# Kernel tuning notes

Hardware: AMD Instinct MI355X
Metric: run time of the kernel (lower is better)

## Reference

```python
import jax, jax.numpy as jnp
import numpy as np

N, D, EDIM, E, K = 10000, 64, 16, 320000, 16


def _lin(key, o, i):
    # kaiming-normal-ish init, std = sqrt(2/fan_in)
    return jax.random.normal(key, (o, i), dtype=jnp.float32) * (2.0 / i) ** 0.5


def setup_inputs() -> dict:
    key = jax.random.key(0)
    ks = jax.random.split(key, 20)
    inp = {
        "x": jax.random.normal(ks[0], (N, D), dtype=jnp.float32),
        "edge_index": jax.random.randint(ks[1], (2, E), 0, N),
        "edge_attr": jax.random.normal(ks[2], (E, EDIM), dtype=jnp.float32),
        "location_info": jax.random.uniform(ks[3], (N, 4), dtype=jnp.float32),
        "k": K,
    }
    i = 4
    for name in ["sg1", "sg2", "sg3"]:
        inp[name + "_wm"] = _lin(ks[i], D, EDIM + D); i += 1
        inp[name + "_bm"] = jnp.zeros((D,), jnp.float32)
        inp[name + "_wu"] = _lin(ks[i], D, D); i += 1
        inp[name + "_bu"] = jnp.zeros((D,), jnp.float32)
    for name in ["dg1", "dg2"]:
        inp[name + "_w1"] = _lin(ks[i], 2 * D, 2 * D); i += 1
        inp[name + "_b1"] = jnp.zeros((2 * D,), jnp.float32)
        inp[name + "_w2"] = _lin(ks[i], D, 2 * D); i += 1
        inp[name + "_b2"] = jnp.zeros((D,), jnp.float32)
    inp["f1_w"] = _lin(ks[i], D, 5 * D); i += 1
    inp["f1_b"] = jnp.zeros((D,), jnp.float32)
    inp["f2_w"] = _lin(ks[i], D, 6 * D); i += 1
    inp["f2_b"] = jnp.zeros((D,), jnp.float32)
    return inp


def _knn_edges(loc, k, n):
    # dynamic kNN on location_info (euclidean, directed src->dst, with self loops)
    loc = jax.lax.stop_gradient(loc)
    d2 = jnp.sum((loc[:, None, :] - loc[None, :, :]) ** 2, axis=-1)  # [N, N]
    d2 = jnp.where(jnp.eye(n, dtype=bool), jnp.inf, d2)
    _, idx = jax.lax.top_k(-d2, k)               # idx[i] = k nearest sources of target i
    dst = jnp.repeat(jnp.arange(n), k)
    src = idx.reshape(-1)
    loops = jnp.arange(n)
    return jnp.concatenate([src, loops]), jnp.concatenate([dst, loops])


def _forward(x, edge_index, edge_attr, location_info, k,
             sg1_wm, sg1_bm, sg1_wu, sg1_bu,
             sg2_wm, sg2_bm, sg2_wu, sg2_bu,
             sg3_wm, sg3_bm, sg3_wu, sg3_bu,
             dg1_w1, dg1_b1, dg1_w2, dg1_b2,
             dg2_w1, dg2_b1, dg2_w2, dg2_b2,
             f1_w, f1_b, f2_w, f2_b):
    n = x.shape[0]
    relu = jax.nn.relu
    s_src, s_dst = edge_index[0], edge_index[1]  # PyG: row=source j, col=target i

    def static_conv(h, wm, bm, wu, bu):
        m = relu(jnp.concatenate([edge_attr, h[s_src] - h[s_dst]], axis=1) @ wm.T + bm)
        agg = jax.ops.segment_max(m, s_dst, num_segments=n)
        agg = jnp.where(jnp.isfinite(agg), agg, 0.0)  # empty segments -> 0
        return relu(agg @ wu.T + bu)

    d_src, d_dst = _knn_edges(location_info, k, n)

    def dyn_conv(h, w1, b1, w2, b2):
        xi = h[d_dst]
        xj = h[d_src]
        m = relu(relu(jnp.concatenate([xi, xj - xi], axis=1) @ w1.T + b1) @ w2.T + b2)
        return jax.ops.segment_max(m, d_dst, num_segments=n)  # self loops => no empty segments

    h1 = static_conv(x, sg1_wm, sg1_bm, sg1_wu, sg1_bu)
    h2 = static_conv(h1, sg2_wm, sg2_bm, sg2_wu, sg2_bu)
    h3 = static_conv(h2, sg3_wm, sg3_bm, sg3_wu, sg3_bu)
    g1 = dyn_conv(h1, dg1_w1, dg1_b1, dg1_w2, dg1_b2)
    g2 = dyn_conv(g1, dg2_w1, dg2_b1, dg2_w2, dg2_b2)

    cat1 = jnp.concatenate([h1, g1, g2, h2, h3], axis=1)        # [N, 5D]
    fuse1 = relu(cat1 @ f1_w.T + f1_b)                          # [N, D]
    cat2 = jnp.concatenate([fuse1, cat1], axis=1)               # [N, 6D]
    return cat2 @ f2_w.T + f2_b                                 # [N, D]


def reference(x, edge_index, edge_attr, location_info, k,
              sg1_wm, sg1_bm, sg1_wu, sg1_bu,
              sg2_wm, sg2_bm, sg2_wu, sg2_bu,
              sg3_wm, sg3_bm, sg3_wu, sg3_bu,
              dg1_w1, dg1_b1, dg1_w2, dg1_b2,
              dg2_w1, dg2_b1, dg2_w2, dg2_b2,
              f1_w, f1_b, f2_w, f2_b):
    return _forward(x, edge_index, edge_attr, location_info, k,
                    sg1_wm, sg1_bm, sg1_wu, sg1_bu,
                    sg2_wm, sg2_bm, sg2_wu, sg2_bu,
                    sg3_wm, sg3_bm, sg3_wu, sg3_bu,
                    dg1_w1, dg1_b1, dg1_w2, dg1_b2,
                    dg2_w1, dg2_b1, dg2_w2, dg2_b2,
                    f1_w, f1_b, f2_w, f2_b)
```

## Files before the change

kernel.cpp:

```cpp
#include <hip/hip_runtime.h>

#define INF_F __builtin_inff()

typedef __attribute__((ext_vector_type(8))) short short8v;
typedef __attribute__((ext_vector_type(4))) float f32x4;
typedef unsigned long long ull;

__device__ __forceinline__ short f2bf(float x) {
  const unsigned u = __float_as_uint(x);
  return (short)((u + 0x7FFFu + ((u >> 16) & 1u)) >> 16);
}

__device__ __forceinline__ unsigned mbcnt64(ull m) {
  return __builtin_amdgcn_mbcnt_hi((unsigned)(m >> 32),
                                   __builtin_amdgcn_mbcnt_lo((unsigned)m, 0u));
}

#define KNN_G 5
#define KNN_NC (KNN_G*KNN_G*KNN_G*KNN_G)
#define KNN_PCAP 1600

__global__ __launch_bounds__(256) void count2_kernel(
    const float* __restrict__ loc, int* __restrict__ cellcount,
    int* __restrict__ cellid, int n,
    const int* __restrict__ dst, int* __restrict__ deg, int E)
{
  const int i = blockIdx.x * 256 + threadIdx.x;
  if (i < n) {
    const float4 l = *(const float4*)(loc + (size_t)i*4);
    const int cx = min(KNN_G-1, (int)(l.x * (float)KNN_G));
    const int cy = min(KNN_G-1, (int)(l.y * (float)KNN_G));
    const int cz = min(KNN_G-1, (int)(l.z * (float)KNN_G));
    const int cw = min(KNN_G-1, (int)(l.w * (float)KNN_G));
    const int c = ((cx*KNN_G + cy)*KNN_G + cz)*KNN_G + cw;
    cellid[i] = c;
    atomicAdd(&cellcount[c], 1);
  }
  if (i < E) atomicAdd(&deg[dst[i]], 1);
}

__device__ __forceinline__ void scan1b_body(
    const int* __restrict__ in, int* __restrict__ out, int n, int per)
{
  __shared__ int part[1024];
  const int t = threadIdx.x;
  const int lo = t * per, hi = min(lo + per, n);
  int sum = 0;
  for (int idx = lo; idx < hi; ++idx) sum += in[idx];
  int v = sum;
  part[t] = v;
  __syncthreads();
  for (int off = 1; off < 1024; off <<= 1) {
    const int o = (t >= off) ? part[t - off] : 0;
    __syncthreads();
    v += o;
    part[t] = v;
    __syncthreads();
  }
  int run = v - sum;
  for (int idx = lo; idx < hi; ++idx) { out[idx] = run; run += in[idx]; }
  if (t == 1023) out[n] = v;
}

__global__ __launch_bounds__(1024) void scan2_kernel(
    const int* __restrict__ inA, int* __restrict__ outA, int nA, int perA,
    const int* __restrict__ inB, int* __restrict__ outB, int nB, int perB)
{
  if (blockIdx.x == 0) scan1b_body(inA, outA, nA, perA);
  else                 scan1b_body(inB, outB, nB, perB);
}

__global__ __launch_bounds__(256) void scatter2_kernel(
    const float* __restrict__ loc, const int* __restrict__ cellid,
    const int* __restrict__ cellstart, int* __restrict__ cellfill,
    float* __restrict__ locs4s, int* __restrict__ oidx, int n,
    const int* __restrict__ srcs, const int* __restrict__ dsts,
    const int* __restrict__ rowptr, int* __restrict__ dfill,
    int* __restrict__ cs_src, int* __restrict__ cs_eid, int E)
{
  const int i = blockIdx.x * 256 + threadIdx.x;
  if (i < n) {
    const int c = cellid[i];
    const int pos = cellstart[c] + atomicAdd(&cellfill[c], 1);
    *(float4*)(locs4s + (size_t)pos*4) = *(const float4*)(loc + (size_t)i*4);
    oidx[pos] = i;
  }
  if (i < E) {
    const int d = dsts[i];
    const int pos = rowptr[d] + atomicAdd(&dfill[d], 1);
    cs_src[pos] = srcs[i];
    cs_eid[pos] = i;
  }
}

__device__ __forceinline__ ull
knn_refine16(ull* __restrict__ B, int cnt, int lane, ull& topsave)
{
  ull v[5];
#pragma unroll
  for (int s = 0; s < 5; ++s) {
    const int idx = lane + 64*s;
    v[s] = (idx < cnt) ? B[idx] : ~0ull;
  }
  ull tau = ~0ull;
#pragma unroll
  for (int r = 0; r < 16; ++r) {
    ull m = v[0]; int sl = 0;
#pragma unroll
    for (int s = 1; s < 5; ++s) if (v[s] < m) { m = v[s]; sl = s; }
    ull mm = m;
#pragma unroll
    for (int off = 32; off >= 1; off >>= 1) {
      const ull o = __shfl_xor(mm, off, 64);
      if (o < mm) mm = o;
    }
    const bool killer = (m == mm);
#pragma unroll
    for (int s = 0; s < 5; ++s) if (killer && sl == s) v[s] = ~0ull;
    if (lane == r) topsave = mm;
    tau = mm;
  }
  if (lane < 16) B[lane] = topsave;
  return tau;
}

__device__ __forceinline__ int
knn_filter(ull* __restrict__ B, int cnt, int lane, ull& tau)
{
  ull v[5];
#pragma unroll
  for (int s = 0; s < 5; ++s) {
    const int idx = lane + 64*s;
    v[s] = (idx < cnt) ? B[idx] : ~0ull;
  }
  ull g = v[0];
#pragma unroll
  for (int s = 1; s < 5; ++s) if (v[s] < g) g = v[s];
  { ull o = __shfl_xor(g, 1, 64); if (o < g) g = o;
    o = __shfl_xor(g, 2, 64); if (o < g) g = o; }
  ull t = g;
#pragma unroll
  for (int off = 4; off <= 32; off <<= 1) {
    const ull o = __shfl_xor(t, off, 64);
    if (o > t) t = o;
  }
  int nc = 0;
#pragma unroll
  for (int s = 0; s < 5; ++s) {
    const bool keep = (v[s] <= t) && (v[s] != ~0ull);
    const ull mask = __ballot(keep);
    if (mask) {
      const unsigned pre = mbcnt64(mask);
      if (keep) B[nc + pre] = v[s];
      nc += (int)__popcll(mask);
    }
  }
  tau = t;
  return nc;
}

__device__ void knn_body(int blk, ull* __restrict__ Bs, int* __restrict__ PosAll,
                         const float* __restrict__ locs4s,
                         const int* __restrict__ oidx,
                         const int* __restrict__ cellstart,
                         int* __restrict__ knn, int n)
{
#pragma clang fp contract(off)
  constexpr int TRIG = 256;
  const int wave = threadIdx.x >> 6, lane = threadIdx.x & 63;
  const int t = blk * 4 + wave;
  if (t >= n) return;
  ull* B = Bs + wave * 320;
  int* Pos = PosAll + wave * KNN_PCAP;

  const float4 L = *(const float4*)(locs4s + (size_t)t*4);
  const float tx = L.x, ty = L.y, tz = L.z, tw = L.w;
  const int cx = min(KNN_G-1, (int)(tx * (float)KNN_G));
  const int cy = min(KNN_G-1, (int)(ty * (float)KNN_G));
  const int cz = min(KNN_G-1, (int)(tz * (float)KNN_G));
  const int cw = min(KNN_G-1, (int)(tw * (float)KNN_G));

  ull tau = ~0ull;
  ull topsave = ~0ull;
  int cnt = 0;

  auto boundB = [&](int mr) -> float {
    const float w = 1.0f / (float)KNN_G;
    float Bv = INF_F;
    if (cx - mr >= 1)         Bv = fminf(Bv, tx - (float)(cx - mr) * w);
    if (cx + mr <= KNN_G - 2) Bv = fminf(Bv, (float)(cx + mr + 1) * w - tx);
    if (cy - mr >= 1)         Bv = fminf(Bv, ty - (float)(cy - mr) * w);
    if (cy + mr <= KNN_G - 2) Bv = fminf(Bv, (float)(cy + mr + 1) * w - ty);
    if (cz - mr >= 1)         Bv = fminf(Bv, tz - (float)(cz - mr) * w);
    if (cz + mr <= KNN_G - 2) Bv = fminf(Bv, (float)(cz + mr + 1) * w - tz);
    if (cw - mr >= 1)         Bv = fminf(Bv, tw - (float)(cw - mr) * w);
    if (cw + mr <= KNN_G - 2) Bv = fminf(Bv, (float)(cw + mr + 1) * w - tw);
    return Bv;
  };

  auto do_range = [&](int ps, int pe) {
    for (int p0 = ps; p0 < pe; p0 += 64) {
      const int p = p0 + lane;
      ull key = ~0ull;
      if (p < pe && p != t) {
        const float4 q = *(const float4*)(locs4s + (size_t)p*4);
        const int oj = oidx[p];
        const float a0 = q.x - tx, a1 = q.y - ty, a2 = q.z - tz, a3 = q.w - tw;
        const float s0 = a0*a0, s1 = a1*a1, s2 = a2*a2, s3 = a3*a3;
        const float d = ((s0 + s1) + s2) + s3;
        key = ((ull)__float_as_uint(d) << 32) | (unsigned)oj;
      }
      const bool surv = key < tau;
      const ull mask = __ballot(surv);
      if (mask) {
        const unsigned pre = mbcnt64(mask);
        if (surv) B[cnt + pre] = key;
        cnt += (int)__popcll(mask);
        if (cnt > TRIG) cnt = knn_filter(B, cnt, lane, tau);
      }
    }
  };

  int psv = 0, pev = 0;
  if (lane < 27) {
    const int cr = (lane == 0) ? 13 : (lane <= 13 ? lane - 1 : lane);
    const int ax = cx + (cr / 9) - 1;
    const int ay = cy + ((cr / 3) % 3) - 1;
    const int az = cz + (cr % 3) - 1;
    if (ax >= 0 && ax < KNN_G && ay >= 0 && ay < KNN_G &&
        az >= 0 && az < KNN_G) {
      const int base = ((ax*KNN_G + ay)*KNN_G + az)*KNN_G;
      const int wlo = max(cw-1, 0), whi = min(cw+1, KNN_G-1);
      psv = cellstart[base + wlo];
      pev = cellstart[base + whi + 1];
    }
  }
  const int len = max(pev - psv, 0);
  int cum = len;
#pragma unroll
  for (int off = 1; off < 64; off <<= 1) {
    const int o = __shfl_up(cum, off, 64);
    if (lane >= off) cum += o;
  }
  const int T = __shfl(cum, 63, 64);
  const int startv = cum - len;

  for (int p = psv, f = startv; p < pev && f < KNN_PCAP; ++p, ++f) Pos[f] = p;

  const int Tb = min(T, KNN_PCAP);
  const int Tm1b = Tb - 1;
  float4 qn; int ojn = 0, pgn = 0; bool vn = false;
  {
    vn = lane < Tb;
    pgn = Pos[min(lane, Tm1b)];
    qn = *(const float4*)(locs4s + (size_t)pgn*4);
    ojn = oidx[pgn];
  }
  for (int f0 = 0; f0 < Tb; f0 += 64) {
    const float4 qc = qn; const int ojc = ojn, pgc = pgn; const bool vc = vn;
    const int fN = f0 + 64 + lane;
    vn = fN < Tb;
    if (f0 + 64 < Tb) {
      pgn = Pos[min(fN, Tm1b)];
      qn = *(const float4*)(locs4s + (size_t)pgn*4);
      ojn = oidx[pgn];
    }
    ull key = ~0ull;
    if (vc && pgc != t) {
      const float a0 = qc.x - tx, a1 = qc.y - ty, a2 = qc.z - tz, a3 = qc.w - tw;
      const float s0 = a0*a0, s1 = a1*a1, s2 = a2*a2, s3 = a3*a3;
      const float d = ((s0 + s1) + s2) + s3;
      key = ((ull)__float_as_uint(d) << 32) | (unsigned)ojc;
    }
    const bool surv = key < tau;
    const ull mask = __ballot(surv);
    if (mask) {
      const unsigned pre = mbcnt64(mask);
      if (surv) B[cnt + pre] = key;
      cnt += (int)__popcll(mask);
      if (cnt > TRIG) cnt = knn_filter(B, cnt, lane, tau);
    }
  }
  if (T > KNN_PCAP) {
    for (int r = 0; r < 27; ++r) {
      const int st = __shfl(startv, r, 64);
      const int ps = __shfl(psv, r, 64);
      const int pe = __shfl(pev, r, 64);
      const int done = min(max(KNN_PCAP - st, 0), pe - ps);
      if (ps + done < pe) do_range(ps + done, pe);
    }
  }

  for (int m = 2; m <= KNN_G - 1; ++m) {
    if (cnt > 16) { tau = knn_refine16(B, cnt, lane, topsave); cnt = 16; }
    if (tau != ~0ull) {
      const float taud = __uint_as_float((unsigned)(tau >> 32));
      const float Bv = boundB(m - 1);
      if (Bv == INF_F || taud < Bv * Bv * 0.99999f) break;
    }
    const int xlo = max(cx-m, 0), xhi = min(cx+m, KNN_G-1);
    for (int ax = xlo; ax <= xhi; ++ax) {
      const bool xe = (ax == cx-m) || (ax == cx+m);
      const int ylo = max(cy-m, 0), yhi = min(cy+m, KNN_G-1);
      for (int ay = ylo; ay <= yhi; ++ay) {
        const bool ye = (ay == cy-m) || (ay == cy+m);
        const int zlo = max(cz-m, 0), zhi = min(cz+m, KNN_G-1);
        for (int az = zlo; az <= zhi; ++az) {
          const bool ze = (az == cz-m) || (az == cz+m);
          const int base = ((ax*KNN_G + ay)*KNN_G + az)*KNN_G;
          if (xe | ye | ze) {
            const int wlo = max(cw-m, 0), whi = min(cw+m, KNN_G-1);
            do_range(cellstart[base+wlo], cellstart[base+whi+1]);
          } else {
            if (cw-m >= 0) {
              const int c = base + cw - m;
              do_range(cellstart[c], cellstart[c+1]);
            }
            if (cw+m <= KNN_G-1) {
              const int c = base + cw + m;
              do_range(cellstart[c], cellstart[c+1]);
            }
          }
        }
      }
    }
  }
  (void)knn_refine16(B, cnt, lane, topsave);
  const int i = oidx[t];
  if (lane < 16) knn[(size_t)i*16 + lane] = (int)(topsave & 0xFFFFFFFFull);
}

__device__ __forceinline__ void stage_tile_bf16(
    short* __restrict__ S, const float* __restrict__ src, int srow, int sc16,
    bool valid)
{
  short tmp[16];
  if (valid) {
#pragma unroll
    for (int u = 0; u < 4; ++u) {
      const float4 v = *(const float4*)(src + u*4);
      tmp[u*4+0] = f2bf(v.x); tmp[u*4+1] = f2bf(v.y);
      tmp[u*4+2] = f2bf(v.z); tmp[u*4+3] = f2bf(v.w);
    }
  } else {
#pragma unroll
    for (int u = 0; u < 16; ++u) tmp[u] = 0;
  }
  *(short8v*)&S[srow*72 + sc16]     = *(short8v*)&tmp[0];
  *(short8v*)&S[srow*72 + sc16 + 8] = *(short8v*)&tmp[8];
}

__global__ __launch_bounds__(256) void mega_kernel(
    const float* __restrict__ locs4s, const int* __restrict__ oidx,
    const int* __restrict__ cellstart, int* __restrict__ knn, int n,
    const float* __restrict__ ea, const int* __restrict__ cs_eid,
    short* __restrict__ eac, int E,
    const float* __restrict__ w1A, const float* __restrict__ b1A,
    float* __restrict__ wpqA, float* __restrict__ bpqA,
    const float* __restrict__ w1B, const float* __restrict__ b1B,
    float* __restrict__ wpqB, float* __restrict__ bpqB,
    const float* __restrict__ x, const float* __restrict__ wm1,
    float* __restrict__ Rout,
    int KB, int EB)
{
  __shared__ __align__(16) char smem[4*320*8 + 4*KNN_PCAP*4];
  const int bid = blockIdx.x;
  if (bid < KB) {
    knn_body(bid, (ull*)smem, (int*)(smem + 4*320*8),
             locs4s, oidx, cellstart, knn, n);
  } else if (bid < KB + EB) {
    const int e = (bid - KB) * 256 + threadIdx.x;
    if (e < E) {
      const float* src = ea + (size_t)cs_eid[e]*16;
      short tmp[16];
#pragma unroll
      for (int u = 0; u < 4; ++u) {
        const float4 v = *(const float4*)(src + u*4);
        tmp[u*4+0] = f2bf(v.x); tmp[u*4+1] = f2bf(v.y);
        tmp[u*4+2] = f2bf(v.z); tmp[u*4+3] = f2bf(v.w);
      }
      *(short8v*)(eac + (size_t)e*16)     = *(short8v*)&tmp[0];
      *(short8v*)(eac + (size_t)e*16 + 8) = *(short8v*)&tmp[8];
    }
  } else if (bid < KB + EB + 64) {
    const int gidx = (bid - KB - EB) * 256 + threadIdx.x;
    const int l = gidx >> 13;
    const int idx = gidx & 8191;
    const float* w1 = l ? w1B : w1A;
    const float* b1 = l ? b1B : b1A;
    float* wpq = l ? wpqB : wpqA;
    float* bpq = l ? bpqB : bpqA;
    const int o = idx >> 6, i = idx & 63;
    const float a = w1[o*128 + i], b = w1[o*128 + 64 + i];
    wpq[idx] = a - b;
    wpq[128*64 + idx] = b;
    if (idx < 128) { bpq[idx] = b1[idx]; bpq[128 + idx] = 0.f; }
  } else {
    short* As = (short*)smem;
    short* Ws = (short*)(smem + 64*72*2);
    const int tid = threadIdx.x;
    const int wave = tid >> 6, lane = tid & 63;
    const int grp = lane >> 4, li = lane & 15;
    const int m0 = (bid - KB - EB - 64) * 64;
    const int srow = tid >> 2;
    const int sc16 = (tid & 3) * 16;
    const int gr = m0 + srow;
    stage_tile_bf16(As, x + (size_t)gr*64 + sc16, srow, sc16, gr < n);
    stage_tile_bf16(Ws, wm1 + (size_t)srow*80 + sc16, srow, sc16, true);
    __syncthreads();
    f32x4 acc[4];
#pragma unroll
    for (int nt = 0; nt < 4; ++nt) acc[nt] = (f32x4)0.f;
#pragma unroll
    for (int ks = 0; ks < 2; ++ks) {
      const short8v a = *(const short8v*)&As[(wave*16 + li)*72 + ks*32 + grp*8];
#pragma unroll
      for (int nt = 0; nt < 4; ++nt) {
        const short8v b = *(const short8v*)&Ws[(nt*16 + li)*72 + ks*32 + grp*8];
        acc[nt] = __builtin_amdgcn_mfma_f32_16x16x32_bf16(a, b, acc[nt], 0, 0, 0);
      }
    }
#pragma unroll
    for (int nt = 0; nt < 4; ++nt) {
      const int ch = nt*16 + li;
#pragma unroll
      for (int j = 0; j < 4; ++j) {
        const int r = m0 + wave*16 + grp*4 + j;
        if (r < n) Rout[(size_t)r*64 + ch] = acc[nt][j];
      }
    }
  }
}

#define TPW_S 2

__global__ __launch_bounds__(256) void static_msg_kernel(
    const float* __restrict__ R, const short* __restrict__ eac,
    const float* __restrict__ wm, const float* __restrict__ bm,
    const int* __restrict__ cs_src, const int* __restrict__ rowptr,
    float* __restrict__ agg, int n)
{
  const int wave = threadIdx.x >> 6, lane = threadIdx.x & 63;
  const int grp = lane >> 4, li = lane & 15;

  short8v bfr[4];
  float bmv[4];
#pragma unroll
  for (int nt = 0; nt < 4; ++nt) {
    short8v b = (short8v)0;
    if (grp < 2) {
      const int ch = nt*16 + li;
#pragma unroll
      for (int j = 0; j < 8; ++j) b[j] = f2bf(wm[ch*80 + grp*8 + j]);
    }
    bfr[nt] = b;
    bmv[nt] = bm[nt*16 + li];
  }
  const f32x4 zero = (f32x4)0.f;

  for (int tg = 0; tg < TPW_S; ++tg) {
    const int d = (blockIdx.x * 4 + wave) * TPW_S + tg;
    if (d >= n) break;
    const int beg = rowptr[d], end = rowptr[d+1];
    const int deg = end - beg;
    float basev[4];
#pragma unroll
    for (int nt = 0; nt < 4; ++nt)
      basev[nt] = bmv[nt] - R[(size_t)d*64 + nt*16 + li];

    float vmax[4] = {0.f, 0.f, 0.f, 0.f};
    for (int m0 = 0; m0 < deg; m0 += 16) {
      short8v a = (short8v)0;
      const int erow = m0 + li;
      if (grp < 2 && erow < deg)
        a = *(const short8v*)(eac + (size_t)(beg + erow)*16 + grp*8);
      f32x4 Dv[4];
#pragma unroll
      for (int nt = 0; nt < 4; ++nt)
        Dv[nt] = __builtin_amdgcn_mfma_f32_16x16x32_bf16(a, bfr[nt], zero, 0, 0, 0);
#pragma unroll
      for (int j = 0; j < 4; ++j) {
        const int m = m0 + grp*4 + j;
        if (m < deg) {
          const int s = cs_src[beg + m];
          const float* Rs = R + (size_t)s*64;
#pragma unroll
          for (int nt = 0; nt < 4; ++nt) {
            const float acc = Dv[nt][j] + Rs[nt*16 + li] + basev[nt];
            vmax[nt] = fmaxf(vmax[nt], fmaxf(acc, 0.f));
          }
        }
      }
    }
#pragma unroll
    for (int nt = 0; nt < 4; ++nt) {
      float m = vmax[nt];
      m = fmaxf(m, __shfl_xor(m, 16, 64));
      m = fmaxf(m, __shfl_xor(m, 32, 64));
      vmax[nt] = m;
    }
    float r = vmax[0];
    r = (grp == 1) ? vmax[1] : r;
    r = (grp == 2) ? vmax[2] : r;
    r = (grp == 3) ? vmax[3] : r;
    agg[(size_t)d*64 + lane] = r;
  }
}

template<bool RELU>
__global__ __launch_bounds__(256) void linear_kernel(
    const float* __restrict__ A, int lda,
    const float* __restrict__ W, int ldw,
    const float* __restrict__ bias,
    float* __restrict__ C, int ldc, int M, int K)
{
  __shared__ short As[64 * 72];
  __shared__ short Ws[64 * 72];
  const int tid = threadIdx.x;
  const int wave = tid >> 6, lane = tid & 63;
  const int grp = lane >> 4, li = lane & 15;
  const int m0 = blockIdx.x * 64;
  const int c0 = blockIdx.y * 64;

  f32x4 acc[4];
#pragma unroll
  for (int nt = 0; nt < 4; ++nt) acc[nt] = (f32x4)0.f;

  const int srow = tid >> 2;
  const int sc16 = (tid & 3) * 16;

  for (int kt = 0; kt < K; kt += 64) {
    const int gr = m0 + srow;
    stage_tile_bf16(As, A + (size_t)gr*lda + kt + sc16, srow, sc16, gr < M);
    stage_tile_bf16(Ws, W + (size_t)(c0 + srow)*ldw + kt + sc16, srow, sc16, true);
    __syncthreads();
#pragma unroll
    for (int ks = 0; ks < 2; ++ks) {
      const short8v a = *(const short8v*)&As[(wave*16 + li)*72 + ks*32 + grp*8];
#pragma unroll
      for (int nt = 0; nt < 4; ++nt) {
        const short8v b = *(const short8v*)&Ws[(nt*16 + li)*72 + ks*32 + grp*8];
        acc[nt] = __builtin_amdgcn_mfma_f32_16x16x32_bf16(a, b, acc[nt], 0, 0, 0);
      }
    }
    __syncthreads();
  }

#pragma unroll
  for (int nt = 0; nt < 4; ++nt) {
    const int ch = c0 + nt*16 + li;
    const float b = bias ? bias[ch] : 0.f;
#pragma unroll
    for (int j = 0; j < 4; ++j) {
      const int gr = m0 + wave*16 + grp*4 + j;
      if (gr < M) {
        float v = acc[nt][j] + b;
        if (RELU) v = fmaxf(v, 0.f);
        C[(size_t)gr*ldc + ch] = v;
      }
    }
  }
}

__global__ __launch_bounds__(256) void fused_hR_kernel(
    const float* __restrict__ A,
    const float* __restrict__ Wu, const float* __restrict__ bu,
    float* __restrict__ Hout, int ldh,
    const float* __restrict__ Wm,
    float* __restrict__ Rout, int M)
{
  __shared__ short As[64 * 72];
  __shared__ short Ws[64 * 72];
  const int tid = threadIdx.x;
  const int wave = tid >> 6, lane = tid & 63;
  const int grp = lane >> 4, li = lane & 15;
  const int m0 = blockIdx.x * 64;
  const int srow = tid >> 2;
  const int sc16 = (tid & 3) * 16;

  {
    const int gr = m0 + srow;
    stage_tile_bf16(As, A + (size_t)gr*64 + sc16, srow, sc16, gr < M);
    stage_tile_bf16(Ws, Wu + (size_t)srow*64 + sc16, srow, sc16, true);
  }
  __syncthreads();
  f32x4 acc[4];
#pragma unroll
  for (int nt = 0; nt < 4; ++nt) acc[nt] = (f32x4)0.f;
#pragma unroll
  for (int ks = 0; ks < 2; ++ks) {
    const short8v a = *(const short8v*)&As[(wave*16 + li)*72 + ks*32 + grp*8];
#pragma unroll
    for (int nt = 0; nt < 4; ++nt) {
      const short8v b = *(const short8v*)&Ws[(nt*16 + li)*72 + ks*32 + grp*8];
      acc[nt] = __builtin_amdgcn_mfma_f32_16x16x32_bf16(a, b, acc[nt], 0, 0, 0);
    }
  }
  __syncthreads();

  stage_tile_bf16(Ws, Wm + (size_t)srow*80 + sc16, srow, sc16, true);
#pragma unroll
  for (int nt = 0; nt < 4; ++nt) {
    const int ch = nt*16 + li;
    const float b = bu[ch];
#pragma unroll
    for (int j = 0; j < 4; ++j) {
      const int row = wave*16 + grp*4 + j;
      const int gr = m0 + row;
      const float v = fmaxf(acc[nt][j] + b, 0.f);
      if (gr < M) Hout[(size_t)gr*ldh + ch] = v;
      As[row*72 + ch] = f2bf(v);
    }
  }
  __syncthreads();

  f32x4 acc2[4];
#pragma unroll
  for (int nt = 0; nt < 4; ++nt) acc2[nt] = (f32x4)0.f;
#pragma unroll
  for (int ks = 0; ks < 2; ++ks) {
    const short8v a = *(const short8v*)&As[(wave*16 + li)*72 + ks*32 + grp*8];
#pragma unroll
    for (int nt = 0; nt < 4; ++nt) {
      const short8v b = *(const short8v*)&Ws[(nt*16 + li)*72 + ks*32 + grp*8];
      acc2[nt] = __builtin_amdgcn_mfma_f32_16x16x32_bf16(a, b, acc2[nt], 0, 0, 0);
    }
  }
#pragma unroll
  for (int nt = 0; nt < 4; ++nt) {
    const int ch = nt*16 + li;
#pragma unroll
    for (int j = 0; j < 4; ++j) {
      const int gr = m0 + wave*16 + grp*4 + j;
      if (gr < M) Rout[(size_t)gr*64 + ch] = acc2[nt][j];
    }
  }
}

__global__ __launch_bounds__(256) void fusion_kernel(
    const float* __restrict__ CAT,
    const float* __restrict__ aggv,
    const float* __restrict__ wu3, const float* __restrict__ bu3,
    const float* __restrict__ f1w, const float* __restrict__ f1b,
    const float* __restrict__ f2w, const float* __restrict__ f2bias,
    float* __restrict__ out, int M)
{
  __shared__ short As[64 * 72];
  __shared__ short W1s[64 * 72];
  __shared__ short W2s[64 * 72];
  __shared__ short H3s[64 * 72];
  const int tid = threadIdx.x;
  const int wave = tid >> 6, lane = tid & 63;
  const int grp = lane >> 4, li = lane & 15;
  const int m0 = blockIdx.x * 64;
  const int srow = tid >> 2;
  const int sc16 = (tid & 3) * 16;

  {
    const int gr = m0 + srow;
    stage_tile_bf16(As,  aggv + (size_t)gr*64 + sc16, srow, sc16, gr < M);
    stage_tile_bf16(W1s, wu3 + (size_t)srow*64 + sc16, srow, sc16, true);
  }
  __syncthreads();
  f32x4 acc1[4], acc2[4];
#pragma unroll
  for (int nt = 0; nt < 4; ++nt) { acc1[nt] = (f32x4)0.f; acc2[nt] = (f32x4)0.f; }
#pragma unroll
  for (int ks = 0; ks < 2; ++ks) {
    const short8v a = *(const short8v*)&As[(wave*16 + li)*72 + ks*32 + grp*8];
#pragma unroll
    for (int nt = 0; nt < 4; ++nt) {
      const short8v b = *(const short8v*)&W1s[(nt*16 + li)*72 + ks*32 + grp*8];
      acc1[nt] = __builtin_amdgcn_mfma_f32_16x16x32_bf16(a, b, acc1[nt], 0, 0, 0);
    }
  }
#pragma unroll
  for (int nt = 0; nt < 4; ++nt) {
    const int ch = nt*16 + li;
    const float b = bu3[ch];
#pragma unroll
    for (int j = 0; j < 4; ++j) {
      const int row = wave*16 + grp*4 + j;
      H3s[row*72 + ch] = f2bf(fmaxf(acc1[nt][j] + b, 0.f));
    }
  }
  __syncthreads();

#pragma unroll
  for (int nt = 0; nt < 4; ++nt) acc1[nt] = (f32x4)0.f;
  for (int tile = 0; tile < 5; ++tile) {
    const int kt = tile * 64;
    if (tile < 4) {
      const int gr = m0 + srow;
      stage_tile_bf16(As, CAT + (size_t)gr*320 + kt + sc16, srow, sc16, gr < M);
    }
    stage_tile_bf16(W1s, f1w + (size_t)srow*320 + kt + sc16, srow, sc16, true);
    stage_tile_bf16(W2s, f2w + (size_t)srow*384 + 64 + kt + sc16, srow, sc16, true);
    __syncthreads();
    const short* Ause = (tile < 4) ? As : H3s;
#pragma unroll
    for (int ks = 0; ks < 2; ++ks) {
      const short8v a = *(const short8v*)&Ause[(wave*16 + li)*72 + ks*32 + grp*8];
#pragma unroll
      for (int nt = 0; nt < 4; ++nt) {
        const short8v b1 = *(const short8v*)&W1s[(nt*16 + li)*72 + ks*32 + grp*8];
        const short8v b2 = *(const short8v*)&W2s[(nt*16 + li)*72 + ks*32 + grp*8];
        acc1[nt] = __builtin_amdgcn_mfma_f32_16x16x32_bf16(a, b1, acc1[nt], 0, 0, 0);
        acc2[nt] = __builtin_amdgcn_mfma_f32_16x16x32_bf16(a, b2, acc2[nt], 0, 0, 0);
      }
    }
    __syncthreads();
  }

  stage_tile_bf16(W1s, f2w + (size_t)srow*384 + sc16, srow, sc16, true);
#pragma unroll
  for (int nt = 0; nt < 4; ++nt) {
    const int ch = nt*16 + li;
    const float b = f1b[ch];
#pragma unroll
    for (int j = 0; j < 4; ++j) {
      const int row = wave*16 + grp*4 + j;
      As[row*72 + ch] = f2bf(fmaxf(acc1[nt][j] + b, 0.f));
    }
  }
  __syncthreads();
#pragma unroll
  for (int ks = 0; ks < 2; ++ks) {
    const short8v a = *(const short8v*)&As[(wave*16 + li)*72 + ks*32 + grp*8];
#pragma unroll
    for (int nt = 0; nt < 4; ++nt) {
      const short8v b = *(const short8v*)&W1s[(nt*16 + li)*72 + ks*32 + grp*8];
      acc2[nt] = __builtin_amdgcn_mfma_f32_16x16x32_bf16(a, b, acc2[nt], 0, 0, 0);
    }
  }
#pragma unroll
  for (int nt = 0; nt < 4; ++nt) {
    const int ch = nt*16 + li;
    const float b = f2bias[ch];
#pragma unroll
    for (int j = 0; j < 4; ++j) {
      const int gr = m0 + wave*16 + grp*4 + j;
      if (gr < M) out[(size_t)gr*64 + ch] = acc2[nt][j] + b;
    }
  }
}

#define TPW 4

__global__ __launch_bounds__(256) void dyn_mfma_kernel(
    const float* __restrict__ PQ,
    const float* __restrict__ W2, const float* __restrict__ b2,
    const int* __restrict__ knn, float* __restrict__ out, int ldo, int n)
{
  __shared__ short w2s[64 * 136];
  __shared__ short Ts[4][17 * 136];
  const int tid = threadIdx.x;
  const int wave = tid >> 6, lane = tid & 63;

  for (int idx = tid; idx < 64 * 128; idx += 256) {
    const int c = idx >> 7, k = idx & 127;
    w2s[c*136 + k] = f2bf(W2[c*128 + k]);
  }
  __syncthreads();

  short8v bfr[4][4];
#pragma unroll
  for (int nt = 0; nt < 4; ++nt)
#pragma unroll
    for (int kt = 0; kt < 4; ++kt)
      bfr[nt][kt] = *(const short8v*)&w2s[(nt*16 + (lane&15))*136 +
                                          kt*32 + (lane>>4)*8];
  const float b2v = b2[lane];
  short* T = Ts[wave];

  for (int tg = 0; tg < TPW; ++tg) {
    const int i = (blockIdx.x * 4 + wave) * TPW + tg;
    if (i >= n) break;
    const size_t i16 = (size_t)i * 16;

    for (int s = 0; s < 9; ++s) {
      const int slot = lane + 64*s;
      if (slot < 544) {
        const int row = slot >> 5, k4 = slot & 31;
        const int j = (row < 16) ? knn[i16 + row] : i;
        const float4 p = *(const float4*)(PQ + (size_t)i*256 + k4*4);
        const float4 q = *(const float4*)(PQ + (size_t)j*256 + 128 + k4*4);
        const float t0 = fmaxf(p.x + q.x, 0.f), t1 = fmaxf(p.y + q.y, 0.f);
        const float t2 = fmaxf(p.z + q.z, 0.f), t3 = fmaxf(p.w + q.w, 0.f);
        int2 w;
        w.x = ((int)(unsigned short)f2bf(t1) << 16) | (unsigned short)f2bf(t0);
        w.y = ((int)(unsigned short)f2bf(t3) << 16) | (unsigned short)f2bf(t2);
        *(int2*)&T[row*136 + k4*4] = w;
      }
    }

    f32x4 acc0[4], acc1[4];
#pragma unroll
    for (int nt = 0; nt < 4; ++nt) {
      acc0[nt] = (f32x4)0.f;
      acc1[nt] = (f32x4)0.f;
    }
#pragma unroll
    for (int kt = 0; kt < 4; ++kt) {
      const short8v a1 = *(const short8v*)&T[(lane&15)*136 + kt*32 + (lane>>4)*8];
      const short8v a2 = *(const short8v*)&T[16*136 + kt*32 + (lane>>4)*8];
#pragma unroll
      for (int nt = 0; nt < 4; ++nt) {
        acc0[nt] = __builtin_amdgcn_mfma_f32_16x16x32_bf16(a1, bfr[nt][kt], acc0[nt], 0, 0, 0);
        acc1[nt] = __builtin_amdgcn_mfma_f32_16x16x32_bf16(a2, bfr[nt][kt], acc1[nt], 0, 0, 0);
      }
    }

    float v[4];
#pragma unroll
    for (int nt = 0; nt < 4; ++nt) {
      float m = fmaxf(fmaxf(acc0[nt][0], acc0[nt][1]),
                      fmaxf(acc0[nt][2], acc0[nt][3]));
      m = fmaxf(m, acc1[nt][0]);
      m = fmaxf(m, __shfl_xor(m, 16, 64));
      m = fmaxf(m, __shfl_xor(m, 32, 64));
      v[nt] = m;
    }
    const int g = lane >> 4;
    float r = v[0];
    r = (g == 1) ? v[1] : r;
    r = (g == 2) ? v[2] : r;
    r = (g == 3) ? v[3] : r;
    out[(size_t)i*ldo + lane] = fmaxf(r + b2v, 0.f);
  }
}

extern "C" void kernel_launch(void* const* d_in, const int* in_sizes, int n_in,
                              void* d_out, int out_size, void* d_ws, size_t ws_size,
                              hipStream_t stream)
{
  const float* x   = (const float*)d_in[0];
  const int*   ei  = (const int*)d_in[1];
  const float* ea  = (const float*)d_in[2];
  const float* loc = (const float*)d_in[3];
  const float* sg_wm[3] = {(const float*)d_in[5],  (const float*)d_in[9],  (const float*)d_in[13]};
  const float* sg_bm[3] = {(const float*)d_in[6],  (const float*)d_in[10], (const float*)d_in[14]};
  const float* sg_wu[3] = {(const float*)d_in[7],  (const float*)d_in[11], (const float*)d_in[15]};
  const float* sg_bu[3] = {(const float*)d_in[8],  (const float*)d_in[12], (const float*)d_in[16]};
  const float* dg_w1[2] = {(const float*)d_in[17], (const float*)d_in[21]};
  const float* dg_b1[2] = {(const float*)d_in[18], (const float*)d_in[22]};
  const float* dg_w2[2] = {(const float*)d_in[19], (const float*)d_in[23]};
  const float* dg_b2[2] = {(const float*)d_in[20], (const float*)d_in[24]};
  const float* f1_w = (const float*)d_in[25];
  const float* f1_b = (const float*)d_in[26];
  const float* f2_w = (const float*)d_in[27];
  const float* f2_b = (const float*)d_in[28];
  float* out = (float*)d_out;

  const int n    = in_sizes[0] / 64;
  const int Etot = in_sizes[1] / 2;
  const int* srcp = ei;
  const int* dstp = ei + Etot;

  char* basep = (char*)d_ws;
  size_t cur = 0;
  auto alloc = [&](size_t bytes) -> void* {
    void* p = basep + cur;
    cur = (cur + bytes + 255) & ~(size_t)255;
    return p;
  };
  float* CAT  = (float*)alloc((size_t)n * 320 * 4);
  float* Rb   = (float*)alloc((size_t)n * 64 * 4);
  float* PQb  = (float*)alloc((size_t)n * 256 * 4);
  float* agg  = (float*)alloc((size_t)n * 64 * 4);
  float* wpq[2];
  float* bpq[2];
  wpq[0] = (float*)alloc(256 * 64 * 4);  bpq[0] = (float*)alloc(256 * 4);
  wpq[1] = (float*)alloc(256 * 64 * 4);  bpq[1] = (float*)alloc(256 * 4);
  int* knnb   = (int*)alloc((size_t)n * 16 * 4);
  int* zeros     = (int*)alloc((size_t)(2*KNN_NC + 2*n) * 4);
  int* cellcount = zeros;
  int* cellfill  = zeros + KNN_NC;
  int* deg       = zeros + 2*KNN_NC;
  int* dfill     = zeros + 2*KNN_NC + n;
  int* cellstart = (int*)alloc((size_t)(KNN_NC + 1) * 4);
  int* cellidb   = (int*)alloc((size_t)n * 4);
  float* locs4s  = (float*)alloc((size_t)n * 4 * 4);
  int* oidx      = (int*)alloc((size_t)n * 4);
  int* rowptr    = (int*)alloc((size_t)(n + 1) * 4);
  int* cs_src    = (int*)alloc((size_t)Etot * 4);
  int* cs_eid    = (int*)alloc((size_t)Etot * 4);
  short* ea_csr  = (short*)alloc((size_t)Etot * 16 * 2);
  (void)ws_size; (void)n_in; (void)out_size;

  const int nbE = (Etot + 255) / 256;
  const int mb = (n + 63) / 64;

  hipMemsetAsync(zeros, 0, (size_t)(2*KNN_NC + 2*n) * 4, stream);
  count2_kernel<<<nbE, 256, 0, stream>>>(loc, cellcount, cellidb, n,
                                         dstp, deg, Etot);
  scan2_kernel<<<2, 1024, 0, stream>>>(cellcount, cellstart, KNN_NC,
                                       (KNN_NC + 1023) / 1024,
                                       deg, rowptr, n, (n + 1023) / 1024);
  scatter2_kernel<<<nbE, 256, 0, stream>>>(loc, cellidb, cellstart, cellfill,
                                           locs4s, oidx, n,
                                           srcp, dstp, rowptr, dfill,
                                           cs_src, cs_eid, Etot);
  const int KB = (n + 3) / 4;
  const int EB = (Etot + 255) / 256;
  mega_kernel<<<KB + EB + 64 + mb, 256, 0, stream>>>(
      locs4s, oidx, cellstart, knnb, n,
      ea, cs_eid, ea_csr, Etot,
      dg_w1[0], dg_b1[0], wpq[0], bpq[0],
      dg_w1[1], dg_b1[1], wpq[1], bpq[1],
      x, sg_wm[0] + 16, Rb,
      KB, EB);

  auto lin = [&](const float* A, int lda, const float* W, int ldw, const float* bias,
                 float* C, int ldc, int K, int ncols, bool relu) {
    dim3 grid(mb, ncols / 64);
    if (relu) linear_kernel<true ><<<grid, 256, 0, stream>>>(A, lda, W, ldw, bias, C, ldc, n, K);
    else      linear_kernel<false><<<grid, 256, 0, stream>>>(A, lda, W, ldw, bias, C, ldc, n, K);
  };

  const int smb = (n + 4*TPW_S - 1) / (4*TPW_S);
  static_msg_kernel<<<smb, 256, 0, stream>>>(Rb, ea_csr, sg_wm[0], sg_bm[0],
                                             cs_src, rowptr, agg, n);
  fused_hR_kernel<<<mb, 256, 0, stream>>>(agg, sg_wu[0], sg_bu[0],
                                          CAT + 0, 320,
                                          sg_wm[1] + 16, Rb, n);
  static_msg_kernel<<<smb, 256, 0, stream>>>(Rb, ea_csr, sg_wm[1], sg_bm[1],
                                             cs_src, rowptr, agg, n);
  fused_hR_kernel<<<mb, 256, 0, stream>>>(agg, sg_wu[1], sg_bu[1],
                                          CAT + 192, 320,
                                          sg_wm[2] + 16, Rb, n);
  static_msg_kernel<<<smb, 256, 0, stream>>>(Rb, ea_csr, sg_wm[2], sg_bm[2],
                                             cs_src, rowptr, agg, n);

  const float* din[2] = {CAT + 0, CAT + 64};
  float* doutp[2] = {CAT + 64, CAT + 128};
  const int db = (n + 4*TPW - 1) / (4*TPW);
  for (int l = 0; l < 2; ++l) {
    lin(din[l], 320, wpq[l], 64, bpq[l], PQb, 256, 64, 256, false);
    dyn_mfma_kernel<<<db, 256, 0, stream>>>(PQb, dg_w2[l], dg_b2[l],
                                            knnb, doutp[l], 320, n);
  }

  fusion_kernel<<<mb, 256, 0, stream>>>(CAT, agg, sg_wu[2], sg_bu[2],
                                        f1_w, f1_b, f2_w, f2_b, out, n);
}
```

Baseline: 295.1 us.

## Fuse static message aggregation into update and fusion GEMM kernels

```diff
diff --git a/kernel.cpp b/kernel.cpp
--- a/kernel.cpp
+++ b/kernel.cpp
@@ -348,6 +348,80 @@
   }
   *(short8v*)&S[srow*72 + sc16]     = *(short8v*)&tmp[0];
   *(short8v*)&S[srow*72 + sc16 + 8] = *(short8v*)&tmp[8];
+}
+
+__device__ __forceinline__ void msg_phase(
+    short* __restrict__ As,
+    const float* __restrict__ R, const short* __restrict__ eac,
+    const short8v* __restrict__ bfr, const float* __restrict__ bmv,
+    const int* __restrict__ cs_src, const int* __restrict__ rowptr,
+    int m0, int wave, int lane, int grp, int li, int M)
+{
+  const f32x4 zero = (f32x4)0.f;
+  for (int tg = 0; tg < 16; ++tg) {
+    const int d = m0 + wave*16 + tg;
+    float vmax[4] = {0.f, 0.f, 0.f, 0.f};
+    if (d < M) {
+      const int beg = rowptr[d], end = rowptr[d+1];
+      const int deg = end - beg;
+      float basev[4];
+#pragma unroll
+      for (int nt = 0; nt < 4; ++nt)
+        basev[nt] = bmv[nt] - R[(size_t)d*64 + nt*16 + li];
+      for (int e0 = 0; e0 < deg; e0 += 16) {
+        short8v a = (short8v)0;
+        const int erow = e0 + li;
+        if (grp < 2 && erow < deg)
+          a = *(const short8v*)(eac + (size_t)(beg + erow)*16 + grp*8);
+        f32x4 Dv[4];
+#pragma unroll
+        for (int nt = 0; nt < 4; ++nt)
+          Dv[nt] = __builtin_amdgcn_mfma_f32_16x16x32_bf16(a, bfr[nt], zero, 0, 0, 0);
+#pragma unroll
+        for (int j = 0; j < 4; ++j) {
+          const int m = e0 + grp*4 + j;
+          if (m < deg) {
+            const int s = cs_src[beg + m];
+            const float* Rs = R + (size_t)s*64;
+#pragma unroll
+            for (int nt = 0; nt < 4; ++nt) {
+              const float acc = Dv[nt][j] + Rs[nt*16 + li] + basev[nt];
+              vmax[nt] = fmaxf(vmax[nt], fmaxf(acc, 0.f));
+            }
+          }
+        }
+      }
+#pragma unroll
+      for (int nt = 0; nt < 4; ++nt) {
+        float mm = vmax[nt];
+        mm = fmaxf(mm, __shfl_xor(mm, 16, 64));
+        mm = fmaxf(mm, __shfl_xor(mm, 32, 64));
+        vmax[nt] = mm;
+      }
+    }
+    float r = vmax[0];
+    r = (grp == 1) ? vmax[1] : r;
+    r = (grp == 2) ? vmax[2] : r;
+    r = (grp == 3) ? vmax[3] : r;
+    As[(wave*16 + tg)*72 + lane] = f2bf(r);
+  }
+}
+
+__device__ __forceinline__ void msg_frags(
+    const float* __restrict__ wm, const float* __restrict__ bm,
+    short8v* __restrict__ bfr, float* __restrict__ bmv, int grp, int li)
+{
+#pragma unroll
+  for (int nt = 0; nt < 4; ++nt) {
+    short8v b = (short8v)0;
+    if (grp < 2) {
+      const int ch = nt*16 + li;
+#pragma unroll
+      for (int j = 0; j < 8; ++j) b[j] = f2bf(wm[ch*80 + grp*8 + j]);
+    }
+    bfr[nt] = b;
+    bmv[nt] = bm[nt*16 + li];
+  }
 }
 
 __global__ __launch_bounds__(256) void mega_kernel(
@@ -432,141 +506,13 @@
   }
 }
 
-#define TPW_S 2
-
-__global__ __launch_bounds__(256) void static_msg_kernel(
+__global__ __launch_bounds__(256) void static_layer_kernel(
     const float* __restrict__ R, const short* __restrict__ eac,
     const float* __restrict__ wm, const float* __restrict__ bm,
     const int* __restrict__ cs_src, const int* __restrict__ rowptr,
-    float* __restrict__ agg, int n)
-{
-  const int wave = threadIdx.x >> 6, lane = threadIdx.x & 63;
-  const int grp = lane >> 4, li = lane & 15;
-
-  short8v bfr[4];
-  float bmv[4];
-#pragma unroll
-  for (int nt = 0; nt < 4; ++nt) {
-    short8v b = (short8v)0;
-    if (grp < 2) {
-      const int ch = nt*16 + li;
-#pragma unroll
-      for (int j = 0; j < 8; ++j) b[j] = f2bf(wm[ch*80 + grp*8 + j]);
-    }
-    bfr[nt] = b;
-    bmv[nt] = bm[nt*16 + li];
-  }
-  const f32x4 zero = (f32x4)0.f;
-
-  for (int tg = 0; tg < TPW_S; ++tg) {
-    const int d = (blockIdx.x * 4 + wave) * TPW_S + tg;
-    if (d >= n) break;
-    const int beg = rowptr[d], end = rowptr[d+1];
-    const int deg = end - beg;
-    float basev[4];
-#pragma unroll
-    for (int nt = 0; nt < 4; ++nt)
-      basev[nt] = bmv[nt] - R[(size_t)d*64 + nt*16 + li];
-
-    float vmax[4] = {0.f, 0.f, 0.f, 0.f};
-    for (int m0 = 0; m0 < deg; m0 += 16) {
-      short8v a = (short8v)0;
-      const int erow = m0 + li;
-      if (grp < 2 && erow < deg)
-        a = *(const short8v*)(eac + (size_t)(beg + erow)*16 + grp*8);
-      f32x4 Dv[4];
-#pragma unroll
-      for (int nt = 0; nt < 4; ++nt)
-        Dv[nt] = __builtin_amdgcn_mfma_f32_16x16x32_bf16(a, bfr[nt], zero, 0, 0, 0);
-#pragma unroll
-      for (int j = 0; j < 4; ++j) {
-        const int m = m0 + grp*4 + j;
-        if (m < deg) {
-          const int s = cs_src[beg + m];
-          const float* Rs = R + (size_t)s*64;
-#pragma unroll
-          for (int nt = 0; nt < 4; ++nt) {
-            const float acc = Dv[nt][j] + Rs[nt*16 + li] + basev[nt];
-            vmax[nt] = fmaxf(vmax[nt], fmaxf(acc, 0.f));
-          }
-        }
-      }
-    }
-#pragma unroll
-    for (int nt = 0; nt < 4; ++nt) {
-      float m = vmax[nt];
-      m = fmaxf(m, __shfl_xor(m, 16, 64));
-      m = fmaxf(m, __shfl_xor(m, 32, 64));
-      vmax[nt] = m;
-    }
-    float r = vmax[0];
-    r = (grp == 1) ? vmax[1] : r;
-    r = (grp == 2) ? vmax[2] : r;
-    r = (grp == 3) ? vmax[3] : r;
-    agg[(size_t)d*64 + lane] = r;
-  }
-}
-
-template<bool RELU>
-__global__ __launch_bounds__(256) void linear_kernel(
-    const float* __restrict__ A, int lda,
-    const float* __restrict__ W, int ldw,
-    const float* __restrict__ bias,
-    float* __restrict__ C, int ldc, int M, int K)
-{
-  __shared__ short As[64 * 72];
-  __shared__ short Ws[64 * 72];
-  const int tid = threadIdx.x;
-  const int wave = tid >> 6, lane = tid & 63;
-  const int grp = lane >> 4, li = lane & 15;
-  const int m0 = blockIdx.x * 64;
-  const int c0 = blockIdx.y * 64;
-
-  f32x4 acc[4];
-#pragma unroll
-  for (int nt = 0; nt < 4; ++nt) acc[nt] = (f32x4)0.f;
-
-  const int srow = tid >> 2;
-  const int sc16 = (tid & 3) * 16;
-
-  for (int kt = 0; kt < K; kt += 64) {
-    const int gr = m0 + srow;
-    stage_tile_bf16(As, A + (size_t)gr*lda + kt + sc16, srow, sc16, gr < M);
-    stage_tile_bf16(Ws, W + (size_t)(c0 + srow)*ldw + kt + sc16, srow, sc16, true);
-    __syncthreads();
-#pragma unroll
-    for (int ks = 0; ks < 2; ++ks) {
-      const short8v a = *(const short8v*)&As[(wave*16 + li)*72 + ks*32 + grp*8];
-#pragma unroll
-      for (int nt = 0; nt < 4; ++nt) {
-        const short8v b = *(const short8v*)&Ws[(nt*16 + li)*72 + ks*32 + grp*8];
-        acc[nt] = __builtin_amdgcn_mfma_f32_16x16x32_bf16(a, b, acc[nt], 0, 0, 0);
-      }
-    }
-    __syncthreads();
-  }
-
-#pragma unroll
-  for (int nt = 0; nt < 4; ++nt) {
-    const int ch = c0 + nt*16 + li;
-    const float b = bias ? bias[ch] : 0.f;
-#pragma unroll
-    for (int j = 0; j < 4; ++j) {
-      const int gr = m0 + wave*16 + grp*4 + j;
-      if (gr < M) {
-        float v = acc[nt][j] + b;
-        if (RELU) v = fmaxf(v, 0.f);
-        C[(size_t)gr*ldc + ch] = v;
-      }
-    }
-  }
-}
-
-__global__ __launch_bounds__(256) void fused_hR_kernel(
-    const float* __restrict__ A,
     const float* __restrict__ Wu, const float* __restrict__ bu,
     float* __restrict__ Hout, int ldh,
-    const float* __restrict__ Wm,
+    const float* __restrict__ Wm_next,
     float* __restrict__ Rout, int M)
 {
   __shared__ short As[64 * 72];
@@ -578,11 +524,11 @@
   const int srow = tid >> 2;
   const int sc16 = (tid & 3) * 16;
 
-  {
-    const int gr = m0 + srow;
-    stage_tile_bf16(As, A + (size_t)gr*64 + sc16, srow, sc16, gr < M);
-    stage_tile_bf16(Ws, Wu + (size_t)srow*64 + sc16, srow, sc16, true);
-  }
+  short8v bfr[4]; float bmv[4];
+  msg_frags(wm, bm, bfr, bmv, grp, li);
+  msg_phase(As, R, eac, bfr, bmv, cs_src, rowptr, m0, wave, lane, grp, li, M);
+
+  stage_tile_bf16(Ws, Wu + (size_t)srow*64 + sc16, srow, sc16, true);
   __syncthreads();
   f32x4 acc[4];
 #pragma unroll
@@ -598,7 +544,7 @@
   }
   __syncthreads();
 
-  stage_tile_bf16(Ws, Wm + (size_t)srow*80 + sc16, srow, sc16, true);
+  stage_tile_bf16(Ws, Wm_next + (size_t)srow*80 + sc16, srow, sc16, true);
 #pragma unroll
   for (int nt = 0; nt < 4; ++nt) {
     const int ch = nt*16 + li;
@@ -637,9 +583,66 @@
   }
 }
 
+template<bool RELU>
+__global__ __launch_bounds__(256) void linear_kernel(
+    const float* __restrict__ A, int lda,
+    const float* __restrict__ W, int ldw,
+    const float* __restrict__ bias,
+    float* __restrict__ C, int ldc, int M, int K)
+{
+  __shared__ short As[64 * 72];
+  __shared__ short Ws[64 * 72];
+  const int tid = threadIdx.x;
+  const int wave = tid >> 6, lane = tid & 63;
+  const int grp = lane >> 4, li = lane & 15;
+  const int m0 = blockIdx.x * 64;
+  const int c0 = blockIdx.y * 64;
+
+  f32x4 acc[4];
+#pragma unroll
+  for (int nt = 0; nt < 4; ++nt) acc[nt] = (f32x4)0.f;
+
+  const int srow = tid >> 2;
+  const int sc16 = (tid & 3) * 16;
+
+  for (int kt = 0; kt < K; kt += 64) {
+    const int gr = m0 + srow;
+    stage_tile_bf16(As, A + (size_t)gr*lda + kt + sc16, srow, sc16, gr < M);
+    stage_tile_bf16(Ws, W + (size_t)(c0 + srow)*ldw + kt + sc16, srow, sc16, true);
+    __syncthreads();
+#pragma unroll
+    for (int ks = 0; ks < 2; ++ks) {
+      const short8v a = *(const short8v*)&As[(wave*16 + li)*72 + ks*32 + grp*8];
+#pragma unroll
+      for (int nt = 0; nt < 4; ++nt) {
+        const short8v b = *(const short8v*)&Ws[(nt*16 + li)*72 + ks*32 + grp*8];
+        acc[nt] = __builtin_amdgcn_mfma_f32_16x16x32_bf16(a, b, acc[nt], 0, 0, 0);
+      }
+    }
+    __syncthreads();
+  }
+
+#pragma unroll
+  for (int nt = 0; nt < 4; ++nt) {
+    const int ch = c0 + nt*16 + li;
+    const float b = bias ? bias[ch] : 0.f;
+#pragma unroll
+    for (int j = 0; j < 4; ++j) {
+      const int gr = m0 + wave*16 + grp*4 + j;
+      if (gr < M) {
+        float v = acc[nt][j] + b;
+        if (RELU) v = fmaxf(v, 0.f);
+        C[(size_t)gr*ldc + ch] = v;
+      }
+    }
+  }
+}
+
 __global__ __launch_bounds__(256) void fusion_kernel(
     const float* __restrict__ CAT,
-    const float* __restrict__ aggv,
+    const float* __restrict__ R3, const short* __restrict__ eac,
+    const float* __restrict__ wm3, const float* __restrict__ bm3,
+    const int* __restrict__ cs_src, const int* __restrict__ rowptr,
     const float* __restrict__ wu3, const float* __restrict__ bu3,
     const float* __restrict__ f1w, const float* __restrict__ f1b,
     const float* __restrict__ f2w, const float* __restrict__ f2bias,
@@ -657,10 +660,12 @@
   const int sc16 = (tid & 3) * 16;
 
   {
-    const int gr = m0 + srow;
-    stage_tile_bf16(As,  aggv + (size_t)gr*64 + sc16, srow, sc16, gr < M);
-    stage_tile_bf16(W1s, wu3 + (size_t)srow*64 + sc16, srow, sc16, true);
-  }
+    short8v bfr[4]; float bmv[4];
+    msg_frags(wm3, bm3, bfr, bmv, grp, li);
+    msg_phase(As, R3, eac, bfr, bmv, cs_src, rowptr, m0, wave, lane, grp, li, M);
+  }
+
+  stage_tile_bf16(W1s, wu3 + (size_t)srow*64 + sc16, srow, sc16, true);
   __syncthreads();
   f32x4 acc1[4], acc2[4];
 #pragma unroll
@@ -866,8 +871,8 @@
   };
   float* CAT  = (float*)alloc((size_t)n * 320 * 4);
   float* Rb   = (float*)alloc((size_t)n * 64 * 4);
+  float* Rb2  = (float*)alloc((size_t)n * 64 * 4);
   float* PQb  = (float*)alloc((size_t)n * 256 * 4);
-  float* agg  = (float*)alloc((size_t)n * 64 * 4);
   float* wpq[2];
   float* bpq[2];
   wpq[0] = (float*)alloc(256 * 64 * 4);  bpq[0] = (float*)alloc(256 * 4);
@@ -918,19 +923,12 @@
     else      linear_kernel<false><<<grid, 256, 0, stream>>>(A, lda, W, ldw, bias, C, ldc, n, K);
   };
 
-  const int smb = (n + 4*TPW_S - 1) / (4*TPW_S);
-  static_msg_kernel<<<smb, 256, 0, stream>>>(Rb, ea_csr, sg_wm[0], sg_bm[0],
-                                             cs_src, rowptr, agg, n);
-  fused_hR_kernel<<<mb, 256, 0, stream>>>(agg, sg_wu[0], sg_bu[0],
-                                          CAT + 0, 320,
-                                          sg_wm[1] + 16, Rb, n);
-  static_msg_kernel<<<smb, 256, 0, stream>>>(Rb, ea_csr, sg_wm[1], sg_bm[1],
-                                             cs_src, rowptr, agg, n);
-  fused_hR_kernel<<<mb, 256, 0, stream>>>(agg, sg_wu[1], sg_bu[1],
-                                          CAT + 192, 320,
-                                          sg_wm[2] + 16, Rb, n);
-  static_msg_kernel<<<smb, 256, 0, stream>>>(Rb, ea_csr, sg_wm[2], sg_bm[2],
-                                             cs_src, rowptr, agg, n);
+  static_layer_kernel<<<mb, 256, 0, stream>>>(
+      Rb, ea_csr, sg_wm[0], sg_bm[0], cs_src, rowptr,
+      sg_wu[0], sg_bu[0], CAT + 0, 320, sg_wm[1] + 16, Rb2, n);
+  static_layer_kernel<<<mb, 256, 0, stream>>>(
+      Rb2, ea_csr, sg_wm[1], sg_bm[1], cs_src, rowptr,
+      sg_wu[1], sg_bu[1], CAT + 192, 320, sg_wm[2] + 16, Rb, n);
 
   const float* din[2] = {CAT + 0, CAT + 64};
   float* doutp[2] = {CAT + 64, CAT + 128};
@@ -941,6 +939,7 @@
                                             knnb, doutp[l], 320, n);
   }
 
-  fusion_kernel<<<mb, 256, 0, stream>>>(CAT, agg, sg_wu[2], sg_bu[2],
-                                        f1_w, f1_b, f2_w, f2_b, out, n);
-}
+  fusion_kernel<<<mb, 256, 0, stream>>>(
+      CAT, Rb, ea_csr, sg_wm[2], sg_bm[2], cs_src, rowptr,
+      sg_wu[2], sg_bu[2], f1_w, f1_b, f2_w, f2_b, out, n);
+}
```

New measurement: 499.7 us. 1.69x slower.
